# Kernel tuning notes

Hardware: AMD Instinct MI355X
Metric: run time of the kernel (lower is better)

Reference implementation:

```python
import jax, jax.numpy as jnp
import numpy as np
import math

B, N, D = 4, 1024, 512
L, H, DH = 6, 8, 64
FF_INNER = 4 * D
NUM_BUCKETS, MAX_DIST = 32, 128
SCALE = 16.0  # cosine_sim_scale
ROT_DIM = 32  # min(32, dim_head)


def layernorm(x, g, stable=False, eps=1e-5):
    if stable:
        x = x / jax.lax.stop_gradient(jnp.max(x, axis=-1, keepdims=True))
    mean = jnp.mean(x, axis=-1, keepdims=True)
    var = jnp.mean(jnp.square(x - mean), axis=-1, keepdims=True)  # unbiased=False
    return (x - mean) * jax.lax.rsqrt(var + eps) * g


def l2norm(x, eps=1e-12):
    return x / jnp.maximum(jnp.linalg.norm(x, axis=-1, keepdims=True), eps)


def rotary_freqs(n):
    inv_freq = 1.0 / (10000.0 ** (jnp.arange(0, ROT_DIM, 2, dtype=jnp.float32) / ROT_DIM))
    f = jnp.arange(n, dtype=jnp.float32)[:, None] * inv_freq[None, :]  # [n, ROT_DIM/2]
    return jnp.repeat(f, 2, axis=-1)  # [n, ROT_DIM], interleaved pairs


def apply_rotary(t, freqs):
    # rotate only first ROT_DIM dims (rotary_embedding_torch semantics)
    rot, passd = t[..., :ROT_DIM], t[..., ROT_DIM:]
    x = rot.reshape(*rot.shape[:-1], ROT_DIM // 2, 2)
    rotated = jnp.stack((-x[..., 1], x[..., 0]), axis=-1).reshape(rot.shape)
    rot = rot * jnp.cos(freqs) + rotated * jnp.sin(freqs)
    return jnp.concatenate([rot, passd], axis=-1)


def rel_pos_bias(emb, i, j):
    # T5-style causal relative position buckets
    rel = jnp.arange(j)[None, :] - jnp.arange(i)[:, None]
    n = jnp.maximum(-rel, 0)
    max_exact = NUM_BUCKETS // 2
    val_large = max_exact + (
        jnp.log(jnp.maximum(n, 1).astype(jnp.float32) / max_exact)
        / math.log(MAX_DIST / max_exact) * (NUM_BUCKETS - max_exact)
    ).astype(jnp.int32)
    val_large = jnp.minimum(val_large, NUM_BUCKETS - 1)
    bucket = jnp.where(n < max_exact, n, val_large)
    return emb[bucket].transpose(2, 0, 1)  # [h, i, j]


def setup_inputs() -> dict:
    key = jax.random.key(0)
    ks = jax.random.split(key, 9)
    s = 0.02
    return {
        "x": jax.random.normal(ks[0], (B, N, D), jnp.float32),
        "rel_pos_emb": jax.random.normal(ks[1], (NUM_BUCKETS, H), jnp.float32) * s,
        "g_attn": jnp.ones((L, D), jnp.float32),
        "null_kv": jax.random.normal(ks[2], (L, 2, DH), jnp.float32),
        "Wq": jax.random.normal(ks[3], (L, D, H * DH), jnp.float32) * s,
        "Wkv": jax.random.normal(ks[4], (L, D, 2 * DH), jnp.float32) * s,
        "Wo": jax.random.normal(ks[5], (L, H * DH, D), jnp.float32) * s,
        "g_attn_out": jnp.ones((L, D), jnp.float32),
        "g_ff": jnp.ones((L, D), jnp.float32),
        "W1": jax.random.normal(ks[6], (L, D, 2 * FF_INNER), jnp.float32) * s,
        "W2": jax.random.normal(ks[7], (L, FF_INNER, D), jnp.float32) * s,
        "g_final": jnp.ones((D,), jnp.float32),
        "W_proj": jax.random.normal(ks[8], (D, D), jnp.float32) * s,
    }


def reference(x, rel_pos_emb, g_attn, null_kv, Wq, Wkv, Wo, g_attn_out, g_ff, W1, W2, g_final, W_proj):
    b, n, d = x.shape
    freqs = rotary_freqs(n)
    bias = rel_pos_bias(rel_pos_emb, n, n + 1)          # [h, n, n+1] (null kv column at j=0)
    causal = jnp.triu(jnp.ones((n, n + 1), dtype=bool), k=2)  # .triu(j - i + 1)
    neg = -jnp.finfo(x.dtype).max
    for l in range(L):
        # --- attention block ---
        xn = layernorm(x, g_attn[l])
        q = (xn @ Wq[l]).reshape(b, n, H, DH).transpose(0, 2, 1, 3) * SCALE  # b h n d
        k, v = jnp.split(xn @ Wkv[l], 2, axis=-1)                            # b n d (single-head kv)
        q = apply_rotary(q, freqs)
        k = apply_rotary(k, freqs)
        k = jnp.concatenate([jnp.broadcast_to(null_kv[l, 0], (b, 1, DH)), k], axis=1)
        v = jnp.concatenate([jnp.broadcast_to(null_kv[l, 1], (b, 1, DH)), v], axis=1)
        qn = l2norm(q) * math.sqrt(SCALE)   # cosine-sim attention
        kn = l2norm(k) * math.sqrt(SCALE)
        sim = jnp.einsum('bhid,bjd->bhij', qn, kn) + bias
        sim = jnp.where(causal, neg, sim)
        attn = jax.nn.softmax(sim.astype(jnp.float32), axis=-1).astype(x.dtype)
        o = jnp.einsum('bhij,bjd->bhid', attn, v).transpose(0, 2, 1, 3).reshape(b, n, H * DH)
        x = x + layernorm(o @ Wo[l], g_attn_out[l])
        # --- SwiGLU feedforward block ---
        hn = layernorm(x, g_ff[l])
        a, gate = jnp.split(hn @ W1[l], 2, axis=-1)
        x = x + (a * jax.nn.silu(gate)) @ W2[l]
    out = layernorm(x, g_final, stable=True)
    return out @ W_proj
```

## Files before the change

kernel.cpp:

```cpp
#include <hip/hip_runtime.h>
#include <hip/hip_bf16.h>
#include <cmath>

using bf16 = __hip_bfloat16;
typedef __bf16 v8bf __attribute__((ext_vector_type(8)));
typedef __bf16 v4bf __attribute__((ext_vector_type(4)));
typedef float  v4f  __attribute__((ext_vector_type(4)));

__device__ __forceinline__ float bf2f(bf16 x) { return __bfloat162float(x); }
__device__ __forceinline__ bf16  f2bf(float x) { return __float2bfloat16(x); }
__device__ __forceinline__ __bf16 tobf(float x) {
    bf16 h = __float2bfloat16(x);
    return __builtin_bit_cast(__bf16, h);
}

__device__ __forceinline__ void gll16(const bf16* g, bf16* l) {
    __builtin_amdgcn_global_load_lds(
        (const __attribute__((address_space(1))) unsigned int*)g,
        (__attribute__((address_space(3))) unsigned int*)l, 16, 0, 0);
}

__device__ __forceinline__ float ldin(const void* p, size_t i, int isf32) {
    if (isf32) return ((const float*)p)[i];
    return bf2f(((const bf16*)p)[i]);
}

__device__ __forceinline__ void ld8(const void* p, size_t base, int f, float v[8]) {
    if (f) {
        const float* pf = (const float*)p + base;
        float4 a = *(const float4*)pf, b = *(const float4*)(pf + 4);
        v[0]=a.x; v[1]=a.y; v[2]=a.z; v[3]=a.w;
        v[4]=b.x; v[5]=b.y; v[6]=b.z; v[7]=b.w;
    } else {
        v8bf a = *(const v8bf*)((const bf16*)p + base);
#pragma unroll
        for (int j = 0; j < 8; ++j) v[j] = (float)a[j];
    }
}

__device__ __forceinline__ float wave_sum(float v) {
#pragma unroll
    for (int o = 32; o > 0; o >>= 1) v += __shfl_xor(v, o, 64);
    return v;
}
__device__ __forceinline__ float wave_max(float v) {
#pragma unroll
    for (int o = 32; o > 0; o >>= 1) v = fmaxf(v, __shfl_xor(v, o, 64));
    return v;
}

__global__ void detect_k(const unsigned short* __restrict__ x, int* __restrict__ flag)
{
    __shared__ int s;
    int t = threadIdx.x;
    if (t == 0) s = 0;
    __syncthreads();
    int bad = 0;
    for (int i = t; i < 4096; i += 256) {
        int e = (x[i] >> 7) & 0xFF;
        if (e >= 147) bad++;
    }
    atomicAdd(&s, bad);
    __syncthreads();
    if (t == 0) *flag = (s > 64) ? 1 : 0;
}


__global__ __launch_bounds__(256)
void gemm_bt_silu(const bf16* __restrict__ A, const bf16* __restrict__ BT,
                  bf16* __restrict__ U, int K, int lda)
{
    __shared__ bf16 As[128 * 32];
    __shared__ bf16 Bs[128 * 32];
    const int t = threadIdx.x;
    const int lane = t & 63;
    const int wave = t >> 6;
    const int wm = (wave >> 1) * 64;
    const int wn = (wave & 1) * 64;
    const int bm = blockIdx.x * 128;
    const int bn = blockIdx.y * 128;
    const int fr = lane & 15;
    const int fk = (((lane >> 4) ^ ((fr >> 1) & 3))) * 8;

    v4f acc[4][4];
#pragma unroll
    for (int i = 0; i < 4; ++i)
#pragma unroll
        for (int j = 0; j < 4; ++j) { v4f z = {0.f, 0.f, 0.f, 0.f}; acc[i][j] = z; }

    for (int k0 = 0; k0 < K; k0 += 32) {
#pragma unroll
        for (int r = 0; r < 2; ++r) {
            int c = t + 256 * r;
            int row = c >> 2;
            int koff = ((c & 3) ^ ((row >> 1) & 3)) * 8;
            gll16(A + (size_t)(bm + row) * lda + k0 + koff, &As[c * 8]);
            gll16(BT + (size_t)(bn + row) * K + k0 + koff, &Bs[c * 8]);
        }
        __syncthreads();
        v8bf af[4], bfr[4];
#pragma unroll
        for (int mt = 0; mt < 4; ++mt)
            af[mt] = *(const v8bf*)(&As[(wm + mt * 16 + fr) * 32 + fk]);
#pragma unroll
        for (int nt = 0; nt < 4; ++nt)
            bfr[nt] = *(const v8bf*)(&Bs[(wn + nt * 16 + fr) * 32 + fk]);
#pragma unroll
        for (int mt = 0; mt < 4; ++mt)
#pragma unroll
            for (int nt = 0; nt < 4; ++nt)
                acc[mt][nt] = __builtin_amdgcn_mfma_f32_16x16x32_bf16(
                    af[mt], bfr[nt], acc[mt][nt], 0, 0, 0);
        __syncthreads();
    }
    const int r0 = (lane >> 4) * 4;
    const int gbase = ((bn + wn) >> 6) * 32;
#pragma unroll
    for (int mt = 0; mt < 4; ++mt)
#pragma unroll
        for (int nt = 0; nt < 2; ++nt)
#pragma unroll
            for (int r = 0; r < 4; ++r) {
                int row = bm + wm + mt * 16 + r0 + r;
                int col = gbase + nt * 16 + fr;
                float a  = acc[mt][nt][r];
                float gg = acc[mt][nt + 2][r];
                U[(size_t)row * 2048 + col] = f2bf(a * (gg / (1.f + __expf(-gg))));
            }
}

__global__ __launch_bounds__(256)
void gemm64(const bf16* __restrict__ A, const bf16* __restrict__ BT,
            bf16* __restrict__ C, int M, int N, int K, int lda)
{
    __shared__ bf16 As[64 * 32];
    __shared__ bf16 Bs[128 * 32];
    const int t = threadIdx.x;
    const int lane = t & 63;
    const int wave = t >> 6;
    const int wm = (wave >> 1) * 32;
    const int wn = (wave & 1) * 64;
    const int bm = blockIdx.x * 64;
    const int bn = blockIdx.y * 128;
    const int fr = lane & 15;
    const int fk = (((lane >> 4) ^ ((fr >> 1) & 3))) * 8;

    v4f acc[2][4];
#pragma unroll
    for (int i = 0; i < 2; ++i)
#pragma unroll
        for (int j = 0; j < 4; ++j) { v4f z = {0.f, 0.f, 0.f, 0.f}; acc[i][j] = z; }

    for (int k0 = 0; k0 < K; k0 += 32) {
        {
            int row = t >> 2;
            int koff = ((t & 3) ^ ((row >> 1) & 3)) * 8;
            gll16(A + (size_t)(bm + row) * lda + k0 + koff, &As[t * 8]);
        }
#pragma unroll
        for (int r = 0; r < 2; ++r) {
            int c = t + 256 * r;
            int row = c >> 2;
            int koff = ((c & 3) ^ ((row >> 1) & 3)) * 8;
            gll16(BT + (size_t)(bn + row) * K + k0 + koff, &Bs[c * 8]);
        }
        __syncthreads();
        v8bf af[2], bfr[4];
#pragma unroll
        for (int mt = 0; mt < 2; ++mt)
            af[mt] = *(const v8bf*)(&As[(wm + mt * 16 + fr) * 32 + fk]);
#pragma unroll
        for (int nt = 0; nt < 4; ++nt)
            bfr[nt] = *(const v8bf*)(&Bs[(wn + nt * 16 + fr) * 32 + fk]);
#pragma unroll
        for (int mt = 0; mt < 2; ++mt)
#pragma unroll
            for (int nt = 0; nt < 4; ++nt)
                acc[mt][nt] = __builtin_amdgcn_mfma_f32_16x16x32_bf16(
                    af[mt], bfr[nt], acc[mt][nt], 0, 0, 0);
        __syncthreads();
    }
    const int r0 = (lane >> 4) * 4;
#pragma unroll
    for (int mt = 0; mt < 2; ++mt)
#pragma unroll
        for (int nt = 0; nt < 4; ++nt)
#pragma unroll
            for (int r = 0; r < 4; ++r) {
                int row = bm + wm + mt * 16 + r0 + r;
                int col = bn + wn + nt * 16 + fr;
                C[(size_t)row * N + col] = f2bf(acc[mt][nt][r]);
            }
}

__global__ __launch_bounds__(256)
void gemm64_out(const bf16* __restrict__ A, const bf16* __restrict__ BT,
                void* __restrict__ C, int M, int N, int K, int lda,
                const int* __restrict__ flag)
{
    __shared__ bf16 As[64 * 32];
    __shared__ bf16 Bs[128 * 32];
    const int f = *flag;
    const int t = threadIdx.x;
    const int lane = t & 63;
    const int wave = t >> 6;
    const int wm = (wave >> 1) * 32;
    const int wn = (wave & 1) * 64;
    const int bm = blockIdx.x * 64;
    const int bn = blockIdx.y * 128;
    const int fr = lane & 15;
    const int fk = (((lane >> 4) ^ ((fr >> 1) & 3))) * 8;

    v4f acc[2][4];
#pragma unroll
    for (int i = 0; i < 2; ++i)
#pragma unroll
        for (int j = 0; j < 4; ++j) { v4f z = {0.f, 0.f, 0.f, 0.f}; acc[i][j] = z; }

    for (int k0 = 0; k0 < K; k0 += 32) {
        {
            int row = t >> 2;
            int koff = ((t & 3) ^ ((row >> 1) & 3)) * 8;
            gll16(A + (size_t)(bm + row) * lda + k0 + koff, &As[t * 8]);
        }
#pragma unroll
        for (int r = 0; r < 2; ++r) {
            int c = t + 256 * r;
            int row = c >> 2;
            int koff = ((c & 3) ^ ((row >> 1) & 3)) * 8;
            gll16(BT + (size_t)(bn + row) * K + k0 + koff, &Bs[c * 8]);
        }
        __syncthreads();
        v8bf af[2], bfr[4];
#pragma unroll
        for (int mt = 0; mt < 2; ++mt)
            af[mt] = *(const v8bf*)(&As[(wm + mt * 16 + fr) * 32 + fk]);
#pragma unroll
        for (int nt = 0; nt < 4; ++nt)
            bfr[nt] = *(const v8bf*)(&Bs[(wn + nt * 16 + fr) * 32 + fk]);
#pragma unroll
        for (int mt = 0; mt < 2; ++mt)
#pragma unroll
            for (int nt = 0; nt < 4; ++nt)
                acc[mt][nt] = __builtin_amdgcn_mfma_f32_16x16x32_bf16(
                    af[mt], bfr[nt], acc[mt][nt], 0, 0, 0);
        __syncthreads();
    }
    const int r0 = (lane >> 4) * 4;
#pragma unroll
    for (int mt = 0; mt < 2; ++mt)
#pragma unroll
        for (int nt = 0; nt < 4; ++nt)
#pragma unroll
            for (int r = 0; r < 4; ++r) {
                int row = bm + wm + mt * 16 + r0 + r;
                int col = bn + wn + nt * 16 + fr;
                if (f) ((float*)C)[(size_t)row * N + col] = acc[mt][nt][r];
                else   ((bf16*)C)[(size_t)row * N + col] = f2bf(acc[mt][nt][r]);
            }
}

__global__ __launch_bounds__(256)
void transpose2_k(const void* __restrict__ in, bf16* __restrict__ out, int R, int C,
                  size_t inZ, size_t outZ, const int* __restrict__ flag)
{
    __shared__ bf16 tile[32][33];
    int f = *flag;
    size_t ioff = (size_t)blockIdx.z * inZ;
    bf16* dst = out + (size_t)blockIdx.z * outZ;
    int c0 = blockIdx.x * 32, r0 = blockIdx.y * 32;
    int tx = threadIdx.x, ty = threadIdx.y;
#pragma unroll
    for (int i = 0; i < 32; i += 8)
        tile[ty + i][tx] = f2bf(ldin(in, ioff + (size_t)(r0 + ty + i) * C + c0 + tx, f));
    __syncthreads();
#pragma unroll
    for (int i = 0; i < 32; i += 8)
        dst[(size_t)(c0 + ty + i) * R + r0 + tx] = tile[tx][ty + i];
}

__global__ __launch_bounds__(256)
void transposeW1_k(const void* __restrict__ in, bf16* __restrict__ out,
                   const int* __restrict__ flag)
{
    __shared__ bf16 tile[32][33];
    int f = *flag;
    size_t ioff = (size_t)blockIdx.z * (512ull * 4096);
    bf16* dst = out + (size_t)blockIdx.z * (512ull * 4096);
    int c0 = blockIdx.x * 32, r0 = blockIdx.y * 32;
    int tx = threadIdx.x, ty = threadIdx.y;
#pragma unroll
    for (int i = 0; i < 32; i += 8)
        tile[ty + i][tx] = f2bf(ldin(in, ioff + (size_t)(r0 + ty + i) * 4096 + c0 + tx, f));
    __syncthreads();
#pragma unroll
    for (int i = 0; i < 32; i += 8) {
        int j = c0 + ty + i;
        int jp = (j < 2048) ? (((j >> 5) << 6) | (j & 31))
                            : ((((j - 2048) >> 5) << 6) | 32 | (j & 31));
        dst[(size_t)jp * 512 + r0 + tx] = tile[tx][ty + i];
    }
}

__global__ __launch_bounds__(256)
void xinit_ln_k(const void* __restrict__ in, const void* __restrict__ g,
                const int* __restrict__ flag, float* __restrict__ x, bf16* __restrict__ xn)
{
    int f = *flag;
    int row = blockIdx.x * 4 + (threadIdx.x >> 6);
    int lane = threadIdx.x & 63;
    int c0 = lane * 8;
    float v[8];
    ld8(in, (size_t)row * 512 + c0, f, v);
    float* xr = x + (size_t)row * 512 + c0;
    *(float4*)xr       = make_float4(v[0], v[1], v[2], v[3]);
    *(float4*)(xr + 4) = make_float4(v[4], v[5], v[6], v[7]);
    float s = 0.f;
#pragma unroll
    for (int j = 0; j < 8; ++j) s += v[j];
    float mean = wave_sum(s) * (1.f / 512.f);
    float q = 0.f;
#pragma unroll
    for (int j = 0; j < 8; ++j) { float d = v[j] - mean; q += d * d; }
    float var = wave_sum(q) * (1.f / 512.f);
    float rstd = rsqrtf(var + 1e-5f);
    float gv[8];
    ld8(g, c0, f, gv);
    v8bf o;
#pragma unroll
    for (int j = 0; j < 8; ++j) o[j] = tobf((v[j] - mean) * rstd * gv[j]);
    *(v8bf*)(xn + (size_t)row * 512 + c0) = o;
}

__global__ __launch_bounds__(256)
void addln_ln_k(const bf16* __restrict__ tin, const void* __restrict__ g1, int g1off,
                const void* __restrict__ g2, int g2off, const int* __restrict__ flag,
                float* __restrict__ x, bf16* __restrict__ xn)
{
    int f = *flag;
    int row = blockIdx.x * 4 + (threadIdx.x >> 6);
    int lane = threadIdx.x & 63;
    int c0 = lane * 8;
    float tv[8];
    {
        v8bf a = *(const v8bf*)(tin + (size_t)row * 512 + c0);
#pragma unroll
        for (int j = 0; j < 8; ++j) tv[j] = (float)a[j];
    }
    float s = 0.f;
#pragma unroll
    for (int j = 0; j < 8; ++j) s += tv[j];
    float mean = wave_sum(s) * (1.f / 512.f);
    float q = 0.f;
#pragma unroll
    for (int j = 0; j < 8; ++j) { float d = tv[j] - mean; q += d * d; }
    float var = wave_sum(q) * (1.f / 512.f);
    float rstd = rsqrtf(var + 1e-5f);
    float g1v[8];
    ld8(g1, (size_t)g1off + c0, f, g1v);
    float* xr = x + (size_t)row * 512 + c0;
    float4 xa = *(float4*)xr, xb = *(float4*)(xr + 4);
    float nx[8] = {xa.x, xa.y, xa.z, xa.w, xb.x, xb.y, xb.z, xb.w};
#pragma unroll
    for (int j = 0; j < 8; ++j) nx[j] += (tv[j] - mean) * rstd * g1v[j];
    *(float4*)xr       = make_float4(nx[0], nx[1], nx[2], nx[3]);
    *(float4*)(xr + 4) = make_float4(nx[4], nx[5], nx[6], nx[7]);
    float s2 = 0.f;
#pragma unroll
    for (int j = 0; j < 8; ++j) s2 += nx[j];
    float mean2 = wave_sum(s2) * (1.f / 512.f);
    float q2 = 0.f;
#pragma unroll
    for (int j = 0; j < 8; ++j) { float e = nx[j] - mean2; q2 += e * e; }
    float var2 = wave_sum(q2) * (1.f / 512.f);
    float rstd2 = rsqrtf(var2 + 1e-5f);
    float g2v[8];
    ld8(g2, (size_t)g2off + c0, f, g2v);
    v8bf o;
#pragma unroll
    for (int j = 0; j < 8; ++j) o[j] = tobf((nx[j] - mean2) * rstd2 * g2v[j]);
    *(v8bf*)(xn + (size_t)row * 512 + c0) = o;
}

__global__ __launch_bounds__(256)
void add_ln_k(const bf16* __restrict__ tin, const void* __restrict__ g, int goff,
              const int* __restrict__ flag, int stable,
              float* __restrict__ x, bf16* __restrict__ xn)
{
    int f = *flag;
    int row = blockIdx.x * 4 + (threadIdx.x >> 6);
    int lane = threadIdx.x & 63;
    int c0 = lane * 8;
    float nx[8];
    {
        v8bf a = *(const v8bf*)(tin + (size_t)row * 512 + c0);
        float* xr = x + (size_t)row * 512 + c0;
        float4 xa = *(float4*)xr, xb = *(float4*)(xr + 4);
        float xv[8] = {xa.x, xa.y, xa.z, xa.w, xb.x, xb.y, xb.z, xb.w};
#pragma unroll
        for (int j = 0; j < 8; ++j) nx[j] = xv[j] + (float)a[j];
        *(float4*)xr       = make_float4(nx[0], nx[1], nx[2], nx[3]);
        *(float4*)(xr + 4) = make_float4(nx[4], nx[5], nx[6], nx[7]);
    }
    float v[8];
#pragma unroll
    for (int j = 0; j < 8; ++j) v[j] = nx[j];
    if (stable) {
        float m = v[0];
#pragma unroll
        for (int j = 1; j < 8; ++j) m = fmaxf(m, v[j]);
        float mx = wave_max(m);
#pragma unroll
        for (int j = 0; j < 8; ++j) v[j] /= mx;
    }
    float s = 0.f;
#pragma unroll
    for (int j = 0; j < 8; ++j) s += v[j];
    float mean = wave_sum(s) * (1.f / 512.f);
    float q = 0.f;
#pragma unroll
    for (int j = 0; j < 8; ++j) { float d = v[j] - mean; q += d * d; }
    float var = wave_sum(q) * (1.f / 512.f);
    float rstd = rsqrtf(var + 1e-5f);
    float gv[8];
    ld8(g, (size_t)goff + c0, f, gv);
    v8bf o;
#pragma unroll
    for (int j = 0; j < 8; ++j) o[j] = tobf((v[j] - mean) * rstd * gv[j]);
    *(v8bf*)(xn + (size_t)row * 512 + c0) = o;
}

__global__ __launch_bounds__(256)
void rotab_k(float2* __restrict__ tab)
{
    int idx = blockIdx.x * 256 + threadIdx.x;
    if (idx >= 16384) return;
    int n = idx >> 4, p = idx & 15;
    float ang = (float)n * expf((float)p * -0.5756462732f);
    tab[idx] = make_float2(cosf(ang), sinf(ang));
}

__global__ __launch_bounds__(256)
void bias_k(const void* __restrict__ rpe, const int* __restrict__ flag, float* __restrict__ tab)
{
    int f = *flag;
    int idx = blockIdx.x * 256 + threadIdx.x;
    if (idx >= 8 * 1025) return;
    int h = idx / 1025, dist = idx % 1025;
    int bkt;
    if (dist < 16) bkt = dist;
    else {
        bkt = 16 + (int)(logf((float)dist / 16.f) / logf(8.f) * 16.f);
        if (bkt > 31) bkt = 31;
    }
    tab[idx] = ldin(rpe, bkt * 8 + h, f) - 16.f;
}

__global__ __launch_bounds__(256)
void qkvprep_k(const bf16* __restrict__ qkv, const void* __restrict__ nkv, int nkoff,
               const int* __restrict__ flag, const float2* __restrict__ rtab,
               bf16* __restrict__ Q, bf16* __restrict__ K, bf16* __restrict__ Vt)
{
    int t = threadIdx.x, lane = t & 63;
    int bid = blockIdx.x;
    if (bid < 2048) {
        int rid = bid * 16 + (t >> 4);
        int h = rid & 7;
        int n = (rid >> 3) & 1023;
        int b = rid >> 13;
        int g16 = t & 15;
        int d0 = g16 * 4;
        v4bf a = *(const v4bf*)(qkv + (size_t)((b << 10) | n) * 640 + h * 64 + d0);
        float v[4];
#pragma unroll
        for (int j = 0; j < 4; ++j) v[j] = (float)a[j] * 16.f;
        if (d0 < 32) {
            float4 cs = *(const float4*)((const float*)rtab + (size_t)n * 32 + (size_t)(d0 >> 1) * 2);
            float r0 = v[0] * cs.x - v[1] * cs.y;
            float r1 = v[1] * cs.x + v[0] * cs.y;
            float r2 = v[2] * cs.z - v[3] * cs.w;
            float r3 = v[3] * cs.z + v[2] * cs.w;
            v[0] = r0; v[1] = r1; v[2] = r2; v[3] = r3;
        }
        float ss = v[0]*v[0] + v[1]*v[1] + v[2]*v[2] + v[3]*v[3];
#pragma unroll
        for (int o = 1; o < 16; o <<= 1) ss += __shfl_xor(ss, o, 64);
        float sc = 4.f / fmaxf(sqrtf(ss), 1e-12f);
        v4bf ov;
#pragma unroll
        for (int j = 0; j < 4; ++j) ov[j] = tobf(v[j] * sc);
        *(v4bf*)(Q + (((size_t)(b * 8 + h)) * 1024 + n) * 64 + d0) = ov;
    } else {
        int f = *flag;
        int rid = (bid - 2048) * 4 + (t >> 6);
        if (rid >= 4 * 1088) return;
        int j = rid % 1088;
        int b = rid / 1088;
        if (j >= 1025) {
            K[((size_t)b * 1088 + j) * 64 + lane] = f2bf(0.f);
            Vt[((size_t)b * 64 + lane) * 1088 + j] = f2bf(0.f);
            return;
        }
        float kv, vv;
        if (j == 0) {
            kv = ldin(nkv, nkoff + lane, f);
            vv = ldin(nkv, nkoff + 64 + lane, f);
        } else {
            int n = j - 1;
            const bf16* src = qkv + (size_t)(b * 1024 + n) * 640 + 512;
            kv = bf2f(src[lane]);
            vv = bf2f(src[64 + lane]);
            if (lane < 32) {
                float2 cs = rtab[n * 16 + (lane >> 1)];
                float other = __shfl_xor(kv, 1, 64);
                float rot = (lane & 1) ? other : -other;
                kv = kv * cs.x + rot * cs.y;
            }
        }
        float nrm = sqrtf(wave_sum(kv * kv));
        kv = kv / fmaxf(nrm, 1e-12f) * 4.f;
        K[((size_t)b * 1088 + j) * 64 + lane] = f2bf(kv);
        Vt[((size_t)b * 64 + lane) * 1088 + j] = f2bf(vv);
    }
}

__global__ __launch_bounds__(256)
void attn_mfma(const bf16* __restrict__ Q, const bf16* __restrict__ Kg,
               const bf16* __restrict__ Vtg, const float* __restrict__ bias,
               bf16* __restrict__ O)
{
    __shared__ bf16 Ks[64][72];
    __shared__ bf16 Vts[64][72];
    __shared__ bf16 Ps[4][16][72];
    __shared__ float bs[1088];
    const int bh = blockIdx.x, b = bh >> 3, h = bh & 7;
    const int yy = (int)gridDim.y - 1 - (int)blockIdx.y;
    const int i0 = yy * 64;
    const int t = threadIdx.x, lane = t & 63, w = t >> 6;
    const int col = lane & 15, quad = lane >> 4, fk = quad * 8;
    const float* bt = bias + h * 1025;
    const bf16* Kb = Kg + (size_t)b * 1088 * 64;
    const bf16* Vb = Vtg + (size_t)b * 64 * 1088;

    for (int idx = t; idx < i0 + 64; idx += 256) bs[idx] = bt[idx];

    v8bf qf[2];
    const bf16* qrow = Q + ((size_t)bh * 1024 + i0 + w * 16 + col) * 64;
    qf[0] = *(const v8bf*)(qrow + fk);
    qf[1] = *(const v8bf*)(qrow + 32 + fk);

    v4f oacc[4];
#pragma unroll
    for (int dt = 0; dt < 4; ++dt) { v4f z = {0.f,0.f,0.f,0.f}; oacc[dt] = z; }
    float lpart[4] = {0.f, 0.f, 0.f, 0.f};

    const int nch = yy + 2;
    const int rr0 = t >> 3, co0 = (t & 7) * 8;
    const int rr1 = (t + 256) >> 3, co1 = co0;

    v8bf kr[2], vr[2];
    {
        kr[0] = *(const v8bf*)(Kb + (size_t)rr0 * 64 + co0);
        vr[0] = *(const v8bf*)(Vb + (size_t)rr0 * 1088 + co0);
        kr[1] = *(const v8bf*)(Kb + (size_t)rr1 * 64 + co1);
        vr[1] = *(const v8bf*)(Vb + (size_t)rr1 * 1088 + co1);
    }

    for (int ch = 0; ch < nch; ++ch) {
        const int j0 = ch * 64;
        __syncthreads();
        *(v8bf*)(&Ks[rr0][co0])  = kr[0];
        *(v8bf*)(&Vts[rr0][co0]) = vr[0];
        *(v8bf*)(&Ks[rr1][co1])  = kr[1];
        *(v8bf*)(&Vts[rr1][co1]) = vr[1];
        if (ch + 1 < nch) {
            int j0n = (ch + 1) * 64;
            kr[0] = *(const v8bf*)(Kb + (size_t)(j0n + rr0) * 64 + co0);
            vr[0] = *(const v8bf*)(Vb + (size_t)rr0 * 1088 + j0n + co0);
            kr[1] = *(const v8bf*)(Kb + (size_t)(j0n + rr1) * 64 + co1);
            vr[1] = *(const v8bf*)(Vb + (size_t)rr1 * 1088 + j0n + co1);
        }
        __syncthreads();

        v4f sreg[4];
#pragma unroll
        for (int nt = 0; nt < 4; ++nt) {
            v4f z = {0.f,0.f,0.f,0.f};
            v8bf kf0 = *(const v8bf*)(&Ks[nt * 16 + col][fk]);
            v8bf kf1 = *(const v8bf*)(&Ks[nt * 16 + col][32 + fk]);
            z = __builtin_amdgcn_mfma_f32_16x16x32_bf16(qf[0], kf0, z, 0, 0, 0);
            z = __builtin_amdgcn_mfma_f32_16x16x32_bf16(qf[1], kf1, z, 0, 0, 0);
            sreg[nt] = z;
        }

        if (ch < yy) {
#pragma unroll
            for (int reg = 0; reg < 4; ++reg) {
                int i = i0 + w * 16 + quad * 4 + reg;
                int dbase = i - j0 - col;
#pragma unroll
                for (int nt = 0; nt < 4; ++nt) {
                    float pp = __expf(sreg[nt][reg] + bs[dbase - nt * 16]);
                    lpart[reg] += pp;
                    Ps[w][quad * 4 + reg][nt * 16 + col] = f2bf(pp);
                }
            }
        } else {
#pragma unroll
            for (int reg = 0; reg < 4; ++reg) {
                int i = i0 + w * 16 + quad * 4 + reg;
#pragma unroll
                for (int nt = 0; nt < 4; ++nt) {
                    int j = j0 + nt * 16 + col;
                    float pp = 0.f;
                    if (j <= i + 1 && j < 1025) {
                        int dist = i - j; if (dist < 0) dist = 0;
                        pp = __expf(sreg[nt][reg] + bs[dist]);
                    }
                    lpart[reg] += pp;
                    Ps[w][quad * 4 + reg][nt * 16 + col] = f2bf(pp);
                }
            }
        }

        v8bf pf[2];
        pf[0] = *(const v8bf*)(&Ps[w][col][fk]);
        pf[1] = *(const v8bf*)(&Ps[w][col][32 + fk]);
#pragma unroll
        for (int dt = 0; dt < 4; ++dt) {
#pragma unroll
            for (int ks = 0; ks < 2; ++ks) {
                v8bf vf = *(const v8bf*)(&Vts[dt * 16 + col][ks * 32 + fk]);
                oacc[dt] = __builtin_amdgcn_mfma_f32_16x16x32_bf16(pf[ks], vf, oacc[dt], 0, 0, 0);
            }
        }
    }

#pragma unroll
    for (int reg = 0; reg < 4; ++reg) {
#pragma unroll
        for (int o = 1; o < 16; o <<= 1) lpart[reg] += __shfl_xor(lpart[reg], o, 64);
        float inv = 1.f / lpart[reg];
        int i = i0 + w * 16 + quad * 4 + reg;
        bf16* orow = O + ((size_t)(b * 1024 + i)) * 512 + h * 64;
#pragma unroll
        for (int dt = 0; dt < 4; ++dt)
            orow[dt * 16 + col] = f2bf(oacc[dt][reg] * inv);
    }
}

extern "C" void kernel_launch(void* const* d_in, const int* in_sizes, int n_in,
                              void* d_out, int out_size, void* d_ws, size_t ws_size,
                              hipStream_t stream)
{
    const void* x_in     = d_in[0];
    const void* rpe      = d_in[1];
    const void* g_attn   = d_in[2];
    const void* null_kv  = d_in[3];
    const void* Wq       = d_in[4];
    const void* Wkv      = d_in[5];
    const void* Wo       = d_in[6];
    const void* g_attn_o = d_in[7];
    const void* g_ff     = d_in[8];
    const void* W1       = d_in[9];
    const void* W2       = d_in[10];
    const void* g_final  = d_in[11];
    const void* W_proj   = d_in[12];

    char* wp = (char*)d_ws;
    auto alloc = [&](size_t bytes) {
        char* p = wp; wp += (bytes + 255) & ~(size_t)255; return p;
    };
    float* xf    = (float*)alloc(4096ull * 512 * 4);
    bf16*  xn    = (bf16*) alloc(4096ull * 512 * 2);
    bf16*  tb    = (bf16*) alloc(4096ull * 512 * 2);
    bf16*  ub    = (bf16*) alloc(4096ull * 4096 * 2);
    bf16*  Kb    = (bf16*) alloc(4ull * 1088 * 64 * 2);
    bf16*  Vtb   = (bf16*) alloc(4ull * 64 * 1088 * 2);
    float* btab  = (float*)alloc(8ull * 1025 * 4);
    float2* rtab = (float2*)alloc(16384ull * 8);
    int*   dfl   = (int*)  alloc(256);
    bf16*  WqkvT = (bf16*) alloc(6ull * 640 * 512 * 2);
    bf16*  WoT   = (bf16*) alloc(6ull * 512 * 512 * 2);
    bf16*  W1T   = (bf16*) alloc(6ull * 4096 * 512 * 2);
    bf16*  W2T   = (bf16*) alloc(6ull * 512 * 2048 * 2);
    bf16*  WpT   = (bf16*) alloc(512ull * 512 * 2);
    bf16*  qkvb  = ub;
    bf16*  Qb    = ub + 2621440;
    bf16*  ob    = ub + 4718592;

    detect_k<<<1, 256, 0, stream>>>((const unsigned short*)x_in, dfl);
    transpose2_k<<<dim3(16, 16, 6),  dim3(32, 8), 0, stream>>>(Wq, WqkvT, 512, 512, 512ull*512, 640ull*512, dfl);
    transpose2_k<<<dim3(4, 16, 6),   dim3(32, 8), 0, stream>>>(Wkv, WqkvT + 512ull*512, 512, 128, 512ull*128, 640ull*512, dfl);
    transpose2_k<<<dim3(16, 16, 6),  dim3(32, 8), 0, stream>>>(Wo, WoT, 512, 512, 512ull*512, 512ull*512, dfl);
    transposeW1_k<<<dim3(128, 16, 6), dim3(32, 8), 0, stream>>>(W1, W1T, dfl);
    transpose2_k<<<dim3(16, 64, 6),  dim3(32, 8), 0, stream>>>(W2, W2T, 2048, 512, 2048ull*512, 2048ull*512, dfl);
    transpose2_k<<<dim3(16, 16, 1),  dim3(32, 8), 0, stream>>>(W_proj, WpT, 512, 512, 512ull*512, 512ull*512, dfl);
    bias_k<<<33, 256, 0, stream>>>(rpe, dfl, btab);
    rotab_k<<<64, 256, 0, stream>>>(rtab);
    xinit_ln_k<<<1024, 256, 0, stream>>>(x_in, g_attn, dfl, xf, xn);

    for (int l = 0; l < 6; ++l) {
        gemm64<<<dim3(64, 5), 256, 0, stream>>>(xn, WqkvT + (size_t)l * 640 * 512, qkvb, 4096, 640, 512, 512);
        qkvprep_k<<<3136, 256, 0, stream>>>(qkvb, null_kv, l * 128, dfl, rtab, Qb, Kb, Vtb);
        attn_mfma<<<dim3(32, 16), 256, 0, stream>>>(Qb, Kb, Vtb, btab, ob);
        gemm64<<<dim3(64, 4), 256, 0, stream>>>(ob, WoT + (size_t)l * 512 * 512, tb, 4096, 512, 512, 512);
        addln_ln_k<<<1024, 256, 0, stream>>>(tb, g_attn_o, l * 512, g_ff, l * 512, dfl, xf, xn);
        gemm_bt_silu<<<dim3(32, 32), 256, 0, stream>>>(xn, W1T + (size_t)l * 4096 * 512, ub, 512, 512);
        gemm64<<<dim3(64, 4), 256, 0, stream>>>(ub, W2T + (size_t)l * 512 * 2048, tb, 4096, 512, 2048, 2048);
        if (l < 5)
            add_ln_k<<<1024, 256, 0, stream>>>(tb, g_attn, (l + 1) * 512, dfl, 0, xf, xn);
        else
            add_ln_k<<<1024, 256, 0, stream>>>(tb, g_final, 0, dfl, 1, xf, xn);
    }
    gemm64_out<<<dim3(64, 4), 256, 0, stream>>>(xn, WpT, d_out, 4096, 512, 512, 512, dfl);
}
```

Before: 936.0 us.

## Use 256x256 double-buffered tiles with 64-wide K steps in SwiGLU GEMM

```diff
diff --git a/kernel.cpp b/kernel.cpp
--- a/kernel.cpp
+++ b/kernel.cpp
@@ -65,58 +65,69 @@
     if (t == 0) *flag = (s > 64) ? 1 : 0;
 }
 
-
-__global__ __launch_bounds__(256)
-void gemm_bt_silu(const bf16* __restrict__ A, const bf16* __restrict__ BT,
+__global__ __launch_bounds__(512, 2)
+void gemm256_silu(const bf16* __restrict__ A, const bf16* __restrict__ BT,
                   bf16* __restrict__ U, int K, int lda)
 {
-    __shared__ bf16 As[128 * 32];
-    __shared__ bf16 Bs[128 * 32];
+    __shared__ bf16 As[2][256 * 64];
+    __shared__ bf16 Bs[2][256 * 64];
     const int t = threadIdx.x;
     const int lane = t & 63;
     const int wave = t >> 6;
-    const int wm = (wave >> 1) * 64;
-    const int wn = (wave & 1) * 64;
-    const int bm = blockIdx.x * 128;
-    const int bn = blockIdx.y * 128;
+    const int wm = (wave >> 2) * 128;
+    const int wn = (wave & 3) * 64;
+    const int bm = blockIdx.x * 256;
+    const int bn = blockIdx.y * 256;
     const int fr = lane & 15;
-    const int fk = (((lane >> 4) ^ ((fr >> 1) & 3))) * 8;
-
-    v4f acc[4][4];
-#pragma unroll
-    for (int i = 0; i < 4; ++i)
+    const int quad = lane >> 4;
+
+    v4f acc[8][4];
+#pragma unroll
+    for (int i = 0; i < 8; ++i)
 #pragma unroll
         for (int j = 0; j < 4; ++j) { v4f z = {0.f, 0.f, 0.f, 0.f}; acc[i][j] = z; }
 
-    for (int k0 = 0; k0 < K; k0 += 32) {
-#pragma unroll
-        for (int r = 0; r < 2; ++r) {
-            int c = t + 256 * r;
-            int row = c >> 2;
-            int koff = ((c & 3) ^ ((row >> 1) & 3)) * 8;
-            gll16(A + (size_t)(bm + row) * lda + k0 + koff, &As[c * 8]);
-            gll16(BT + (size_t)(bn + row) * K + k0 + koff, &Bs[c * 8]);
+    auto stage = [&](int buf, int k0) {
+#pragma unroll
+        for (int r = 0; r < 4; ++r) {
+            int c = t + 512 * r;
+            int row = c >> 3;
+            int g = (c & 7) ^ (row & 7);
+            gll16(A + (size_t)(bm + row) * lda + k0 + g * 8, &As[buf][c * 8]);
+            gll16(BT + (size_t)(bn + row) * K + k0 + g * 8, &Bs[buf][c * 8]);
+        }
+    };
+
+    stage(0, 0);
+    __syncthreads();
+    const int nb = K >> 6;
+    for (int kt = 0; kt < nb; ++kt) {
+        const int buf = kt & 1;
+        if (kt + 1 < nb) stage(buf ^ 1, (kt + 1) * 64);
+#pragma unroll
+        for (int ks = 0; ks < 2; ++ks) {
+            v8bf af[8], bfr[4];
+            const int gk = ((ks * 4 + quad) ^ (fr & 7)) * 8;
+#pragma unroll
+            for (int mt = 0; mt < 8; ++mt)
+                af[mt] = *(const v8bf*)(&As[buf][(wm + mt * 16 + fr) * 64 + gk]);
+#pragma unroll
+            for (int nt = 0; nt < 4; ++nt)
+                bfr[nt] = *(const v8bf*)(&Bs[buf][(wn + nt * 16 + fr) * 64 + gk]);
+#pragma unroll
+            for (int mt = 0; mt < 8; ++mt)
+#pragma unroll
+                for (int nt = 0; nt < 4; ++nt)
+                    acc[mt][nt] = __builtin_amdgcn_mfma_f32_16x16x32_bf16(
+                        af[mt], bfr[nt], acc[mt][nt], 0, 0, 0);
         }
         __syncthreads();
-        v8bf af[4], bfr[4];
-#pragma unroll
-        for (int mt = 0; mt < 4; ++mt)
-            af[mt] = *(const v8bf*)(&As[(wm + mt * 16 + fr) * 32 + fk]);
-#pragma unroll
-        for (int nt = 0; nt < 4; ++nt)
-            bfr[nt] = *(const v8bf*)(&Bs[(wn + nt * 16 + fr) * 32 + fk]);
-#pragma unroll
-        for (int mt = 0; mt < 4; ++mt)
-#pragma unroll
-            for (int nt = 0; nt < 4; ++nt)
-                acc[mt][nt] = __builtin_amdgcn_mfma_f32_16x16x32_bf16(
-                    af[mt], bfr[nt], acc[mt][nt], 0, 0, 0);
-        __syncthreads();
-    }
-    const int r0 = (lane >> 4) * 4;
+    }
+
+    const int r0 = quad * 4;
     const int gbase = ((bn + wn) >> 6) * 32;
 #pragma unroll
-    for (int mt = 0; mt < 4; ++mt)
+    for (int mt = 0; mt < 8; ++mt)
 #pragma unroll
         for (int nt = 0; nt < 2; ++nt)
 #pragma unroll
@@ -128,6 +139,7 @@
                 U[(size_t)row * 2048 + col] = f2bf(a * (gg / (1.f + __expf(-gg))));
             }
 }
+
 
 __global__ __launch_bounds__(256)
 void gemm64(const bf16* __restrict__ A, const bf16* __restrict__ BT,
@@ -706,7 +718,7 @@
         attn_mfma<<<dim3(32, 16), 256, 0, stream>>>(Qb, Kb, Vtb, btab, ob);
         gemm64<<<dim3(64, 4), 256, 0, stream>>>(ob, WoT + (size_t)l * 512 * 512, tb, 4096, 512, 512, 512);
         addln_ln_k<<<1024, 256, 0, stream>>>(tb, g_attn_o, l * 512, g_ff, l * 512, dfl, xf, xn);
-        gemm_bt_silu<<<dim3(32, 32), 256, 0, stream>>>(xn, W1T + (size_t)l * 4096 * 512, ub, 512, 512);
+        gemm256_silu<<<dim3(16, 16), 512, 0, stream>>>(xn, W1T + (size_t)l * 4096 * 512, ub, 512, 512);
         gemm64<<<dim3(64, 4), 256, 0, stream>>>(ub, W2T + (size_t)l * 512 * 2048, tb, 4096, 512, 2048, 2048);
         if (l < 5)
             add_ln_k<<<1024, 256, 0, stream>>>(tb, g_attn, (l + 1) * 512, dfl, 0, xf, xn);
```

After: 896.0 us. 1.04x faster.
